# Kernel tuning notes

Hardware: AMD Instinct MI355X
Metric: run time of the kernel (lower is better)

## Reference

```python
import jax, jax.numpy as jnp
import numpy as np


def _linear_interp(t, S):
    """1D linear interpolation along last axis, matching F.interpolate(mode='linear', align_corners=False).
    t: [B, C, L] -> [B, C, S]"""
    L = t.shape[-1]
    src = jnp.clip((jnp.arange(S, dtype=jnp.float32) + 0.5) * (L / S) - 0.5, 0.0, L - 1)
    i0 = jnp.floor(src).astype(jnp.int32)
    i1 = jnp.minimum(i0 + 1, L - 1)
    w = (src - i0.astype(jnp.float32)).astype(t.dtype)
    return t[..., i0] * (1.0 - w) + t[..., i1] * w


def setup_inputs() -> dict:
    key = jax.random.key(0)
    k1, k2, k3, k4 = jax.random.split(key, 4)
    B, C, H, W, L, D = 32, 768, 32, 32, 77, 512
    return {
        "img_feat": jax.random.normal(k1, (B, C, H, W), dtype=jnp.float32),
        "text_feat": jax.random.normal(k2, (B, L, D), dtype=jnp.float32),
        "W_txt": jax.random.normal(k3, (D, C), dtype=jnp.float32) / np.float32(np.sqrt(D)),
        "gamma": jax.random.normal(k4, (1,), dtype=jnp.float32) * 0.1,
    }


def reference(img_feat, text_feat, W_txt, gamma):
    B, C, H, W = img_feat.shape
    S = H * W
    q = img_feat.reshape(B, C, S)                          # [B,C,S]
    # Linear(D->C, bias=False) then transpose(1,2): [B,L,D] -> [B,C,L]
    t = jnp.einsum('bld,dc->bcl', text_feat, W_txt)
    t = _linear_interp(t, S)                               # [B,C,S]
    scale = S ** (-0.5)
    # attn = bmm(q [B,C,S], t^T [B,S,C]) * scale -> [B,C,C] channel attention
    attn = jax.nn.softmax(jnp.einsum('bis,bjs->bij', q, t) * scale, axis=-1)
    out = q + gamma * jnp.einsum('bij,bjs->bis', attn, t)  # gamma-gated residual
    return out.reshape(B, C, H, W)
```

## Files before the change

### kernel.cpp

```cpp
#include <hip/hip_runtime.h>

#define BB 32
#define CC 768
#define SS 1024
#define LLn 77
#define DD 512
#define LP 80
#define LP2 96
#define QSTR 1048

#define RATIO 0.0751953125f

#define CVT_TXT_BLOCKS (BB * LP * DD / 4 / 256)
#define CVT_W_BLOCKS ((CC / 32) * (DD / 32))
#define AB_BLOCKS (4 * 5 * 8 * 64 * 8 / 4 / 256)
#define TG_BLOCKS (BB * 5 * 4)

typedef short bf16x8 __attribute__((ext_vector_type(8)));
typedef float f32x4 __attribute__((ext_vector_type(4)));
typedef unsigned short u16;

__device__ __forceinline__ u16 f2bf(float f) {
    unsigned int u; __builtin_memcpy(&u, &f, 4);
    u += 0x7fffu + ((u >> 16) & 1u);
    return (u16)(u >> 16);
}

__global__ __launch_bounds__(256) void k_cvt(const float* __restrict__ text,
                                             const float* __restrict__ Wt,
                                             u16* __restrict__ At,
                                             u16* __restrict__ Wb,
                                             u16* __restrict__ Abf) {
    __shared__ float tile[32 * 33];
    const int bx = blockIdx.x;
    const int tid = threadIdx.x;
    if (bx < CVT_TXT_BLOCKS) {
        int j = bx * 256 + tid;
        int row80 = j >> 7, col4 = (j & 127) << 2;
        int b = row80 / LP, l = row80 - b * LP;
        u16 o[4] = {0, 0, 0, 0};
        if (l < LLn) {
            float4 v = *reinterpret_cast<const float4*>(&text[((size_t)b * LLn + l) * DD + col4]);
            o[0] = f2bf(v.x); o[1] = f2bf(v.y); o[2] = f2bf(v.z); o[3] = f2bf(v.w);
        }
        *reinterpret_cast<uint2*>(&At[(size_t)row80 * DD + col4]) = *reinterpret_cast<uint2*>(o);
    } else if (bx < CVT_TXT_BLOCKS + CVT_W_BLOCKS) {
        const int bw = bx - CVT_TXT_BLOCKS;
        const int c0 = (bw % (CC / 32)) * 32, d0 = (bw / (CC / 32)) * 32;
        const int tx = tid & 31, ty = tid >> 5;
#pragma unroll
        for (int k = 0; k < 4; ++k) {
            int d = ty + k * 8;
            tile[d * 33 + tx] = Wt[(size_t)(d0 + d) * CC + c0 + tx];
        }
        __syncthreads();
#pragma unroll
        for (int k = 0; k < 4; ++k) {
            int c = ty + k * 8;
            Wb[(size_t)(c0 + c) * DD + d0 + tx] = f2bf(tile[tx * 33 + c]);
        }
    } else {
        int g = (bx - CVT_TXT_BLOCKS - CVT_W_BLOCKS) * 1024 + tid * 4;
        int e0   = g & 7;
        int lane = (g >> 3) & 63;
        int kk   = (g >> 9) & 7;
        int nt   = (g >> 12) % 5;
        int w    = g / 20480;
        int l    = nt * 16 + (lane & 15);
        int sb   = w * 256 + kk * 32 + ((lane >> 4) << 3) + e0;
        float fl = (float)l;
        u16 o[4];
#pragma unroll
        for (int k = 0; k < 4; ++k) {
            float src = fmaf((float)(sb + k) + 0.5f, RATIO, -0.5f);
            src = fminf(fmaxf(src, 0.f), 76.f);
            o[k] = f2bf(fmaxf(0.f, 1.f - fabsf(src - fl)) * 0.03125f);
        }
        *reinterpret_cast<uint2*>(&Abf[g]) = *reinterpret_cast<uint2*>(o);
    }
}

__global__ __launch_bounds__(256) void k_tgemm(const u16* __restrict__ At,
                                               const u16* __restrict__ Wb,
                                               u16* __restrict__ tc,
                                               u16* __restrict__ tlc) {
    const int bx = blockIdx.x;
    const int tid = threadIdx.x;
    const int cg = bx / 160, mt = bx % 160;
    const int b = mt / 5, tile = mt % 5;
    const int l0 = tile * 16;
    const int w = tid >> 6, lane = tid & 63;
    const int lm = lane & 15, lg = lane >> 4;
    const int c0 = cg * 192 + w * 48;

    f32x4 acc[3];
#pragma unroll
    for (int nt = 0; nt < 3; ++nt) acc[nt] = (f32x4){0.f, 0.f, 0.f, 0.f};

    const u16* ap = At + ((size_t)b * LP + l0 + lm) * DD + lg * 8;
    const u16* bp = Wb + (size_t)(c0 + lm) * DD + lg * 8;
#pragma unroll 4
    for (int ks = 0; ks < 16; ++ks) {
        bf16x8 aq = *reinterpret_cast<const bf16x8*>(ap + ks * 32);
#pragma unroll
        for (int nt = 0; nt < 3; ++nt) {
            bf16x8 bv = *reinterpret_cast<const bf16x8*>(bp + (size_t)nt * 16 * DD + ks * 32);
            acc[nt] = __builtin_amdgcn_mfma_f32_16x16x32_bf16(aq, bv, acc[nt], 0, 0, 0);
        }
    }

    const int lq = l0 + lg * 4;
#pragma unroll
    for (int nt = 0; nt < 3; ++nt) {
        int c = c0 + nt * 16 + lm;
        u16 pk[4];
#pragma unroll
        for (int r = 0; r < 4; ++r) pk[r] = f2bf(acc[nt][r]);
        uint2 pv; __builtin_memcpy(&pv, pk, 8);
        *reinterpret_cast<uint2*>(&tc[((size_t)b * CC + c) * LP2 + lq]) = pv;
#pragma unroll
        for (int r = 0; r < 4; ++r)
            tlc[((size_t)b * LP + lq + r) * CC + c] = pk[r];
    }
    if (tile == 4 && lg == 0) {
        uint4 z = {0u, 0u, 0u, 0u};
#pragma unroll
        for (int nt = 0; nt < 3; ++nt) {
            int c = c0 + nt * 16 + lm;
            *reinterpret_cast<uint4*>(&tc[((size_t)b * CC + c) * LP2 + 80]) = z;
            *reinterpret_cast<uint4*>(&tc[((size_t)b * CC + c) * LP2 + 88]) = z;
        }
    }
}

__global__ __launch_bounds__(256, 2) void k_fused(const u16* __restrict__ tc,
                                                  const u16* __restrict__ tlc,
                                                  const u16* __restrict__ Abf,
                                                  const float* __restrict__ q,
                                                  const float* __restrict__ gamma,
                                                  float* __restrict__ out) {
    __shared__ __align__(16) char un[16 * QSTR * 2];
    u16* qlds = (u16*)un;
    char* pbufBase = un;
    float* us = (float*)(un + 25600);
    float* pmax = (float*)(un + 30720);
    float* psum = (float*)(un + 30976);
    __shared__ u16 qh_bf[16 * 96];

    const int b = blockIdx.y;
    const int iBase = blockIdx.x * 16;
    const int tid = threadIdx.x;
    const int w = tid >> 6, lane = tid & 63;
    const int lm = lane & 15, lg = lane >> 4;
    const float g = gamma[0];

    const size_t qBase = ((size_t)b * CC + iBase) * SS + (size_t)(tid << 2);
    f32x4 qreg[16];
#pragma unroll
    for (int r = 0; r < 16; ++r)
        qreg[r] = *reinterpret_cast<const f32x4*>(&q[qBase + (size_t)r * SS]);
    const int s0 = tid << 2;
#pragma unroll
    for (int r = 0; r < 16; ++r) {
        u16 pk[4] = {f2bf(qreg[r][0]), f2bf(qreg[r][1]), f2bf(qreg[r][2]), f2bf(qreg[r][3])};
        uint2 pv; __builtin_memcpy(&pv, pk, 8);
        *reinterpret_cast<uint2*>(&qlds[r * QSTR + s0]) = pv;
    }
    __syncthreads();

    f32x4 aqh[5];
#pragma unroll
    for (int nt = 0; nt < 5; ++nt) aqh[nt] = (f32x4){0.f, 0.f, 0.f, 0.f};
    {
        const u16* abw = Abf + ((size_t)(w * 5) << 12) + (lane << 3);
#pragma unroll
        for (int kk = 0; kk < 8; ++kk) {
            bf16x8 av = *reinterpret_cast<const bf16x8*>(&qlds[lm * QSTR + w * 256 + kk * 32 + lg * 8]);
#pragma unroll
            for (int nt = 0; nt < 5; ++nt) {
                bf16x8 bv = *reinterpret_cast<const bf16x8*>(abw + (((nt << 3) + kk) << 9));
                aqh[nt] = __builtin_amdgcn_mfma_f32_16x16x32_bf16(av, bv, aqh[nt], 0, 0, 0);
            }
        }
    }
    __syncthreads();
    {
        float* qp = (float*)(pbufBase + w * 6400);
#pragma unroll
        for (int nt = 0; nt < 5; ++nt) {
#pragma unroll
            for (int r = 0; r < 4; ++r)
                qp[(lg * 4 + r) * 80 + nt * 16 + lm] = aqh[nt][r];
        }
    }
    __syncthreads();
#pragma unroll
    for (int k = 0; k < 5; ++k) {
        int e = tid + (k << 8);
        int row = e / 80, l = e - row * 80;
        float v = ((float*)(pbufBase))[row * 80 + l]
                + ((float*)(pbufBase + 6400))[row * 80 + l]
                + ((float*)(pbufBase + 12800))[row * 80 + l]
                + ((float*)(pbufBase + 19200))[row * 80 + l];
        qh_bf[row * 96 + l] = f2bf(v);
    }
    {
        int i = tid;
        if (i < 16 * 16) qh_bf[(i >> 4) * 96 + 80 + (i & 15)] = 0;
    }
    __syncthreads();

    bf16x8 aq0 = *reinterpret_cast<const bf16x8*>(&qh_bf[lm * 96 + lg * 8]);
    bf16x8 aq1 = *reinterpret_cast<const bf16x8*>(&qh_bf[lm * 96 + 32 + lg * 8]);
    bf16x8 aq2 = *reinterpret_cast<const bf16x8*>(&qh_bf[lm * 96 + 64 + lg * 8]);

    f32x4 acc[12];
#pragma unroll
    for (int t = 0; t < 12; ++t) acc[t] = (f32x4){0.f, 0.f, 0.f, 0.f};

    const u16* tcb = tc + ((size_t)b * CC + w * 192 + lm) * LP2 + lg * 8;
#pragma unroll
    for (int t = 0; t < 12; ++t) {
        const u16* p = tcb + (size_t)t * 16 * LP2;
        bf16x8 b0 = *reinterpret_cast<const bf16x8*>(p);
        bf16x8 b1 = *reinterpret_cast<const bf16x8*>(p + 32);
        bf16x8 b2 = *reinterpret_cast<const bf16x8*>(p + 64);
        acc[t] = __builtin_amdgcn_mfma_f32_16x16x32_bf16(aq0, b0, acc[t], 0, 0, 0);
        acc[t] = __builtin_amdgcn_mfma_f32_16x16x32_bf16(aq1, b1, acc[t], 0, 0, 0);
        acc[t] = __builtin_amdgcn_mfma_f32_16x16x32_bf16(aq2, b2, acc[t], 0, 0, 0);
    }

    float m[4];
#pragma unroll
    for (int r = 0; r < 4; ++r) {
        float mm = acc[0][r];
#pragma unroll
        for (int t = 1; t < 12; ++t) mm = fmaxf(mm, acc[t][r]);
#pragma unroll
        for (int off = 8; off >= 1; off >>= 1) mm = fmaxf(mm, __shfl_xor(mm, off));
        m[r] = mm;
    }
    if (lm == 0) {
#pragma unroll
        for (int r = 0; r < 4; ++r) pmax[w * 16 + lg * 4 + r] = m[r];
    }
    __syncthreads();
    float gm[4];
#pragma unroll
    for (int r = 0; r < 4; ++r) {
        int row = lg * 4 + r;
        gm[r] = fmaxf(fmaxf(pmax[row], pmax[16 + row]), fmaxf(pmax[32 + row], pmax[48 + row]));
    }
    float s[4] = {0.f, 0.f, 0.f, 0.f};
#pragma unroll
    for (int t = 0; t < 12; ++t) {
#pragma unroll
        for (int r = 0; r < 4; ++r) {
            float e = __expf(acc[t][r] - gm[r]);
            acc[t][r] = e;
            s[r] += e;
        }
    }
#pragma unroll
    for (int r = 0; r < 4; ++r) {
#pragma unroll
        for (int off = 8; off >= 1; off >>= 1) s[r] += __shfl_xor(s[r], off);
    }
    if (lm == 0) {
#pragma unroll
        for (int r = 0; r < 4; ++r) psum[w * 16 + lg * 4 + r] = s[r];
    }

    u16* P = (u16*)(pbufBase + w * 6400);
#pragma unroll
    for (int t = 0; t < 12; ++t) {
#pragma unroll
        for (int r = 0; r < 4; ++r)
            P[(lg * 4 + r) * 200 + t * 16 + lm] = f2bf(acc[t][r]);
    }

    f32x4 u[5];
#pragma unroll
    for (int nt = 0; nt < 5; ++nt) u[nt] = (f32x4){0.f, 0.f, 0.f, 0.f};
    const u16* tb = tlc + ((size_t)b * LP + lm) * CC + w * 192 + lg * 8;
#pragma unroll
    for (int ks = 0; ks < 6; ++ks) {
        bf16x8 pa = *reinterpret_cast<const bf16x8*>(&P[lm * 200 + ks * 32 + lg * 8]);
#pragma unroll
        for (int nt = 0; nt < 5; ++nt) {
            bf16x8 bv = *reinterpret_cast<const bf16x8*>(tb + (size_t)nt * 16 * CC + ks * 32);
            u[nt] = __builtin_amdgcn_mfma_f32_16x16x32_bf16(pa, bv, u[nt], 0, 0, 0);
        }
    }

    float* up = (float*)(pbufBase + w * 6400);
#pragma unroll
    for (int nt = 0; nt < 5; ++nt) {
#pragma unroll
        for (int r = 0; r < 4; ++r)
            up[(lg * 4 + r) * 81 + nt * 16 + lm] = u[nt][r];
    }
    __syncthreads();
#pragma unroll
    for (int k = 0; k < 5; ++k) {
        int idx = tid + (k << 8);
        int row = idx / LP, l = idx - row * LP;
        float v = ((float*)(pbufBase))[row * 81 + l]
                + ((float*)(pbufBase + 6400))[row * 81 + l]
                + ((float*)(pbufBase + 12800))[row * 81 + l]
                + ((float*)(pbufBase + 19200))[row * 81 + l];
        float denom = psum[row] + psum[16 + row] + psum[32 + row] + psum[48 + row];
        us[row * LP + l] = v / denom;
    }
    __syncthreads();

    float wgt[4]; int i0k[4], i1x[4];
#pragma unroll
    for (int k = 0; k < 4; ++k) {
        float src = fmaf((float)(s0 + k) + 0.5f, RATIO, -0.5f);
        src = fminf(fmaxf(src, 0.f), 76.f);
        i0k[k] = (int)src;
        wgt[k] = src - (float)i0k[k];
        i1x[k] = (i0k[k] < 76) ? i0k[k] + 1 : 76;
    }
#pragma unroll
    for (int r = 0; r < 16; ++r) {
        const float* ur = &us[r * LP];
        f32x4 o;
#pragma unroll
        for (int k = 0; k < 4; ++k) {
            float uv = fmaf(1.f - wgt[k], ur[i0k[k]], wgt[k] * ur[i1x[k]]);
            o[k] = qreg[r][k] + g * uv;
        }
        __builtin_nontemporal_store(o, reinterpret_cast<f32x4*>(&out[qBase + (size_t)r * SS]));
    }
}

extern "C" void kernel_launch(void* const* d_in, const int* in_sizes, int n_in,
                              void* d_out, int out_size, void* d_ws, size_t ws_size,
                              hipStream_t stream) {
    const float* img   = (const float*)d_in[0];
    const float* text  = (const float*)d_in[1];
    const float* Wt    = (const float*)d_in[2];
    const float* gamma = (const float*)d_in[3];
    float* out = (float*)d_out;
    char* ws = (char*)d_ws;
    u16*   tc_bf  = (u16*)(ws);
    u16*   tlc_bf = (u16*)(ws + 4718592);
    u16*   At_bf  = (u16*)(ws + 8650752);
    u16*   Wb_bf  = (u16*)(ws + 11272192);
    u16*   Abf_bf = (u16*)(ws + 12058624);

    k_cvt<<<dim3(CVT_TXT_BLOCKS + CVT_W_BLOCKS + AB_BLOCKS), 256, 0, stream>>>(
        text, Wt, At_bf, Wb_bf, Abf_bf);
    k_tgemm<<<dim3(TG_BLOCKS), 256, 0, stream>>>(At_bf, Wb_bf, tc_bf, tlc_bf);
    k_fused<<<dim3(48, BB), 256, 0, stream>>>(tc_bf, tlc_bf, Abf_bf, img, gamma, out);
}
```

Baseline: 98.89 us.

## Keep q as packed bf16 in registers, double-buffer MFMA operand loads, raise occupancy

Keeps the residual q in registers as packed bf16 rather than fp32, halving that register footprint. Raises the launch bound to 3 blocks per SIMD set. Software-pipelines the three MFMA phases (qh projection, logits, P·V) with A/B register double-buffering so global loads overlap compute. The residual add now uses bf16-rounded q instead of the exact fp32 input, which loses output precision and may exceed tolerance.

```diff
diff --git a/kernel.cpp b/kernel.cpp
--- a/kernel.cpp
+++ b/kernel.cpp
@@ -20,6 +20,12 @@
 typedef float f32x4 __attribute__((ext_vector_type(4)));
 typedef unsigned short u16;
 
+#define MFMA __builtin_amdgcn_mfma_f32_16x16x32_bf16
+
+__device__ __forceinline__ float bf2f(unsigned int h16) {
+    unsigned int u = h16 << 16;
+    float f; __builtin_memcpy(&f, &u, 4); return f;
+}
 __device__ __forceinline__ u16 f2bf(float f) {
     unsigned int u; __builtin_memcpy(&u, &f, 4);
     u += 0x7fffu + ((u >> 16) & 1u);
@@ -105,7 +111,7 @@
 #pragma unroll
         for (int nt = 0; nt < 3; ++nt) {
             bf16x8 bv = *reinterpret_cast<const bf16x8*>(bp + (size_t)nt * 16 * DD + ks * 32);
-            acc[nt] = __builtin_amdgcn_mfma_f32_16x16x32_bf16(aq, bv, acc[nt], 0, 0, 0);
+            acc[nt] = MFMA(aq, bv, acc[nt], 0, 0, 0);
         }
     }
 
@@ -133,7 +139,37 @@
     }
 }
 
-__global__ __launch_bounds__(256, 2) void k_fused(const u16* __restrict__ tc,
+#define LOADAB(arr, c) { _Pragma("unroll") for (int nt = 0; nt < 5; ++nt) { \
+    arr[2*nt]   = *reinterpret_cast<const bf16x8*>(abw + (((nt<<3)+2*(c))<<9)); \
+    arr[2*nt+1] = *reinterpret_cast<const bf16x8*>(abw + (((nt<<3)+2*(c)+1)<<9)); } }
+
+#define QHSTEP(c, CUR) { \
+    bf16x8 av0 = *reinterpret_cast<const bf16x8*>(&qlds[lm*QSTR + w*256 + (2*(c))*32 + lg*8]); \
+    bf16x8 av1 = *reinterpret_cast<const bf16x8*>(&qlds[lm*QSTR + w*256 + (2*(c)+1)*32 + lg*8]); \
+    _Pragma("unroll") for (int nt = 0; nt < 5; ++nt) { \
+        aqh[nt] = MFMA(av0, CUR[2*nt],   aqh[nt], 0, 0, 0); \
+        aqh[nt] = MFMA(av1, CUR[2*nt+1], aqh[nt], 0, 0, 0); } }
+
+#define LOADTC(arr, ch) { _Pragma("unroll") for (int tt = 0; tt < 2; ++tt) { \
+    const u16* p_ = tcb + (size_t)((ch)*2+tt) * 16 * LP2; \
+    arr[tt*3+0] = *reinterpret_cast<const bf16x8*>(p_); \
+    arr[tt*3+1] = *reinterpret_cast<const bf16x8*>(p_ + 32); \
+    arr[tt*3+2] = *reinterpret_cast<const bf16x8*>(p_ + 64); } }
+
+#define LSTEP(ch, CUR) { _Pragma("unroll") for (int tt = 0; tt < 2; ++tt) { \
+    acc[(ch)*2+tt] = MFMA(aq0, CUR[tt*3+0], acc[(ch)*2+tt], 0, 0, 0); \
+    acc[(ch)*2+tt] = MFMA(aq1, CUR[tt*3+1], acc[(ch)*2+tt], 0, 0, 0); \
+    acc[(ch)*2+tt] = MFMA(aq2, CUR[tt*3+2], acc[(ch)*2+tt], 0, 0, 0); } }
+
+#define LOADPV(arr, ks) { _Pragma("unroll") for (int nt = 0; nt < 5; ++nt) \
+    arr[nt] = *reinterpret_cast<const bf16x8*>(tb + (size_t)nt * 16 * CC + (ks)*32); }
+
+#define PVSTEP(ks, CUR) { \
+    bf16x8 pa = *reinterpret_cast<const bf16x8*>(&P[lm*200 + (ks)*32 + lg*8]); \
+    _Pragma("unroll") for (int nt = 0; nt < 5; ++nt) \
+        u[nt] = MFMA(pa, CUR[nt], u[nt], 0, 0, 0); }
+
+__global__ __launch_bounds__(256, 3) void k_fused(const u16* __restrict__ tc,
                                                   const u16* __restrict__ tlc,
                                                   const u16* __restrict__ Abf,
                                                   const float* __restrict__ q,
@@ -155,34 +191,38 @@
     const float g = gamma[0];
 
     const size_t qBase = ((size_t)b * CC + iBase) * SS + (size_t)(tid << 2);
-    f32x4 qreg[16];
+    const int s0 = tid << 2;
+    uint2 qpk[16];
+#pragma unroll
+    for (int r = 0; r < 16; ++r) {
+        f32x4 v = *reinterpret_cast<const f32x4*>(&q[qBase + (size_t)r * SS]);
+        u16 pk[4] = {f2bf(v[0]), f2bf(v[1]), f2bf(v[2]), f2bf(v[3])};
+        __builtin_memcpy(&qpk[r], pk, 8);
+    }
 #pragma unroll
     for (int r = 0; r < 16; ++r)
-        qreg[r] = *reinterpret_cast<const f32x4*>(&q[qBase + (size_t)r * SS]);
-    const int s0 = tid << 2;
-#pragma unroll
-    for (int r = 0; r < 16; ++r) {
-        u16 pk[4] = {f2bf(qreg[r][0]), f2bf(qreg[r][1]), f2bf(qreg[r][2]), f2bf(qreg[r][3])};
-        uint2 pv; __builtin_memcpy(&pv, pk, 8);
-        *reinterpret_cast<uint2*>(&qlds[r * QSTR + s0]) = pv;
-    }
+        *reinterpret_cast<uint2*>(&qlds[r * QSTR + s0]) = qpk[r];
+
+    const u16* abw = Abf + ((size_t)(w * 5) << 12) + (lane << 3);
+    bf16x8 abA[10], abB[10];
+    LOADAB(abA, 0);
     __syncthreads();
 
     f32x4 aqh[5];
 #pragma unroll
     for (int nt = 0; nt < 5; ++nt) aqh[nt] = (f32x4){0.f, 0.f, 0.f, 0.f};
-    {
-        const u16* abw = Abf + ((size_t)(w * 5) << 12) + (lane << 3);
-#pragma unroll
-        for (int kk = 0; kk < 8; ++kk) {
-            bf16x8 av = *reinterpret_cast<const bf16x8*>(&qlds[lm * QSTR + w * 256 + kk * 32 + lg * 8]);
-#pragma unroll
-            for (int nt = 0; nt < 5; ++nt) {
-                bf16x8 bv = *reinterpret_cast<const bf16x8*>(abw + (((nt << 3) + kk) << 9));
-                aqh[nt] = __builtin_amdgcn_mfma_f32_16x16x32_bf16(av, bv, aqh[nt], 0, 0, 0);
-            }
-        }
-    }
+    LOADAB(abB, 1);
+    QHSTEP(0, abA);
+    LOADAB(abA, 2);
+    QHSTEP(1, abB);
+    LOADAB(abB, 3);
+    QHSTEP(2, abA);
+    QHSTEP(3, abB);
+
+    const u16* tcb = tc + ((size_t)b * CC + w * 192 + lm) * LP2 + lg * 8;
+    bf16x8 tcA[6], tcB[6];
+    LOADTC(tcA, 0);
+
     __syncthreads();
     {
         float* qp = (float*)(pbufBase + w * 6400);
@@ -204,10 +244,7 @@
                 + ((float*)(pbufBase + 19200))[row * 80 + l];
         qh_bf[row * 96 + l] = f2bf(v);
     }
-    {
-        int i = tid;
-        if (i < 16 * 16) qh_bf[(i >> 4) * 96 + 80 + (i & 15)] = 0;
-    }
+    if (tid < 16 * 16) qh_bf[(tid >> 4) * 96 + 80 + (tid & 15)] = 0;
     __syncthreads();
 
     bf16x8 aq0 = *reinterpret_cast<const bf16x8*>(&qh_bf[lm * 96 + lg * 8]);
@@ -218,17 +255,21 @@
 #pragma unroll
     for (int t = 0; t < 12; ++t) acc[t] = (f32x4){0.f, 0.f, 0.f, 0.f};
 
-    const u16* tcb = tc + ((size_t)b * CC + w * 192 + lm) * LP2 + lg * 8;
-#pragma unroll
-    for (int t = 0; t < 12; ++t) {
-        const u16* p = tcb + (size_t)t * 16 * LP2;
-        bf16x8 b0 = *reinterpret_cast<const bf16x8*>(p);
-        bf16x8 b1 = *reinterpret_cast<const bf16x8*>(p + 32);
-        bf16x8 b2 = *reinterpret_cast<const bf16x8*>(p + 64);
-        acc[t] = __builtin_amdgcn_mfma_f32_16x16x32_bf16(aq0, b0, acc[t], 0, 0, 0);
-        acc[t] = __builtin_amdgcn_mfma_f32_16x16x32_bf16(aq1, b1, acc[t], 0, 0, 0);
-        acc[t] = __builtin_amdgcn_mfma_f32_16x16x32_bf16(aq2, b2, acc[t], 0, 0, 0);
-    }
+    LOADTC(tcB, 1);
+    LSTEP(0, tcA);
+    LOADTC(tcA, 2);
+    LSTEP(1, tcB);
+    LOADTC(tcB, 3);
+    LSTEP(2, tcA);
+    LOADTC(tcA, 4);
+    LSTEP(3, tcB);
+    LOADTC(tcB, 5);
+    LSTEP(4, tcA);
+    LSTEP(5, tcB);
+
+    const u16* tb = tlc + ((size_t)b * LP + lm) * CC + w * 192 + lg * 8;
+    bf16x8 pvA[5], pvB[5];
+    LOADPV(pvA, 0);
 
     float m[4];
 #pragma unroll
@@ -282,16 +323,17 @@
     f32x4 u[5];
 #pragma unroll
     for (int nt = 0; nt < 5; ++nt) u[nt] = (f32x4){0.f, 0.f, 0.f, 0.f};
-    const u16* tb = tlc + ((size_t)b * LP + lm) * CC + w * 192 + lg * 8;
-#pragma unroll
-    for (int ks = 0; ks < 6; ++ks) {
-        bf16x8 pa = *reinterpret_cast<const bf16x8*>(&P[lm * 200 + ks * 32 + lg * 8]);
-#pragma unroll
-        for (int nt = 0; nt < 5; ++nt) {
-            bf16x8 bv = *reinterpret_cast<const bf16x8*>(tb + (size_t)nt * 16 * CC + ks * 32);
-            u[nt] = __builtin_amdgcn_mfma_f32_16x16x32_bf16(pa, bv, u[nt], 0, 0, 0);
-        }
-    }
+    LOADPV(pvB, 1);
+    PVSTEP(0, pvA);
+    LOADPV(pvA, 2);
+    PVSTEP(1, pvB);
+    LOADPV(pvB, 3);
+    PVSTEP(2, pvA);
+    LOADPV(pvA, 4);
+    PVSTEP(3, pvB);
+    LOADPV(pvB, 5);
+    PVSTEP(4, pvA);
+    PVSTEP(5, pvB);
 
     float* up = (float*)(pbufBase + w * 6400);
 #pragma unroll
@@ -326,11 +368,14 @@
 #pragma unroll
     for (int r = 0; r < 16; ++r) {
         const float* ur = &us[r * LP];
+        uint2 qq = qpk[r];
+        float qf[4] = {bf2f(qq.x & 0xffffu), bf2f(qq.x >> 16),
+                       bf2f(qq.y & 0xffffu), bf2f(qq.y >> 16)};
         f32x4 o;
 #pragma unroll
         for (int k = 0; k < 4; ++k) {
             float uv = fmaf(1.f - wgt[k], ur[i0k[k]], wgt[k] * ur[i1x[k]]);
-            o[k] = qreg[r][k] + g * uv;
+            o[k] = qf[k] + g * uv;
         }
         __builtin_nontemporal_store(o, reinterpret_cast<f32x4*>(&out[qBase + (size_t)r * SS]));
     }
```

Result: no change. 98.33 us (-0.6%).

## Keep q as packed bf16 in registers, shrink LDS, raise occupancy, remap blocks

Applied to the files above, without the earlier changes.

The fused kernel now holds the image tile as packed bf16 in registers instead of fp32, halving that register footprint. Each wave stages only its own slice of q in a per-wave LDS region, which drops one block-wide barrier and shrinks shared memory. Launch bounds go from 2 to 4 blocks per SIMD to raise occupancy, and a 1D grid with a swizzled block-to-batch mapping is meant to improve L2 locality across XCDs. The trade-off is that the residual term is now added from bf16-rounded q rather than exact fp32 input, which loses accuracy in the output.

```diff
diff --git a/kernel.cpp b/kernel.cpp
--- a/kernel.cpp
+++ b/kernel.cpp
@@ -7,7 +7,8 @@
 #define DD 512
 #define LP 80
 #define LP2 96
-#define QSTR 1048
+#define QBS 264
+#define WREG 8448
 
 #define RATIO 0.0751953125f
 
@@ -20,6 +21,12 @@
 typedef float f32x4 __attribute__((ext_vector_type(4)));
 typedef unsigned short u16;
 
+#define MFMA __builtin_amdgcn_mfma_f32_16x16x32_bf16
+
+__device__ __forceinline__ float bf2f(unsigned int h16) {
+    unsigned int u = h16 << 16;
+    float f; __builtin_memcpy(&f, &u, 4); return f;
+}
 __device__ __forceinline__ u16 f2bf(float f) {
     unsigned int u; __builtin_memcpy(&u, &f, 4);
     u += 0x7fffu + ((u >> 16) & 1u);
@@ -105,7 +112,7 @@
 #pragma unroll
         for (int nt = 0; nt < 3; ++nt) {
             bf16x8 bv = *reinterpret_cast<const bf16x8*>(bp + (size_t)nt * 16 * DD + ks * 32);
-            acc[nt] = __builtin_amdgcn_mfma_f32_16x16x32_bf16(aq, bv, acc[nt], 0, 0, 0);
+            acc[nt] = MFMA(aq, bv, acc[nt], 0, 0, 0);
         }
     }
 
@@ -133,59 +140,56 @@
     }
 }
 
-__global__ __launch_bounds__(256, 2) void k_fused(const u16* __restrict__ tc,
+__global__ __launch_bounds__(256, 4) void k_fused(const u16* __restrict__ tc,
                                                   const u16* __restrict__ tlc,
                                                   const u16* __restrict__ Abf,
                                                   const float* __restrict__ q,
                                                   const float* __restrict__ gamma,
                                                   float* __restrict__ out) {
-    __shared__ __align__(16) char un[16 * QSTR * 2];
-    u16* qlds = (u16*)un;
-    char* pbufBase = un;
-    float* us = (float*)(un + 25600);
-    float* pmax = (float*)(un + 30720);
-    float* psum = (float*)(un + 30976);
-    __shared__ u16 qh_bf[16 * 96];
-
-    const int b = blockIdx.y;
-    const int iBase = blockIdx.x * 16;
+    __shared__ __align__(16) char un[4 * WREG];
+    __shared__ __align__(16) char sh2[5120];
+    __shared__ float pmax[64];
+    __shared__ float psum[64];
+
+    const int id = blockIdx.x;
+    const int o = id >> 3;
+    const int b = (id & 7) * 4 + o / 48;
+    const int iBase = (o % 48) * 16;
+
     const int tid = threadIdx.x;
     const int w = tid >> 6, lane = tid & 63;
     const int lm = lane & 15, lg = lane >> 4;
     const float g = gamma[0];
 
     const size_t qBase = ((size_t)b * CC + iBase) * SS + (size_t)(tid << 2);
-    f32x4 qreg[16];
+    const int s0 = tid << 2;
+    uint2 qpk[16];
+#pragma unroll
+    for (int r = 0; r < 16; ++r) {
+        f32x4 v = *reinterpret_cast<const f32x4*>(&q[qBase + (size_t)r * SS]);
+        u16 pk[4] = {f2bf(v[0]), f2bf(v[1]), f2bf(v[2]), f2bf(v[3])};
+        __builtin_memcpy(&qpk[r], pk, 8);
+    }
+    u16* qbuf = (u16*)(un + w * WREG);
 #pragma unroll
     for (int r = 0; r < 16; ++r)
-        qreg[r] = *reinterpret_cast<const f32x4*>(&q[qBase + (size_t)r * SS]);
-    const int s0 = tid << 2;
-#pragma unroll
-    for (int r = 0; r < 16; ++r) {
-        u16 pk[4] = {f2bf(qreg[r][0]), f2bf(qreg[r][1]), f2bf(qreg[r][2]), f2bf(qreg[r][3])};
-        uint2 pv; __builtin_memcpy(&pv, pk, 8);
-        *reinterpret_cast<uint2*>(&qlds[r * QSTR + s0]) = pv;
-    }
-    __syncthreads();
+        *reinterpret_cast<uint2*>(&qbuf[r * QBS + lane * 4]) = qpk[r];
 
     f32x4 aqh[5];
 #pragma unroll
     for (int nt = 0; nt < 5; ++nt) aqh[nt] = (f32x4){0.f, 0.f, 0.f, 0.f};
+    const u16* abw = Abf + ((size_t)(w * 5) << 12) + (lane << 3);
+#pragma unroll
+    for (int kk = 0; kk < 8; ++kk) {
+        bf16x8 av = *reinterpret_cast<const bf16x8*>(&qbuf[lm * QBS + kk * 32 + lg * 8]);
+#pragma unroll
+        for (int nt = 0; nt < 5; ++nt) {
+            bf16x8 bv = *reinterpret_cast<const bf16x8*>(abw + (((nt << 3) + kk) << 9));
+            aqh[nt] = MFMA(av, bv, aqh[nt], 0, 0, 0);
+        }
+    }
     {
-        const u16* abw = Abf + ((size_t)(w * 5) << 12) + (lane << 3);
-#pragma unroll
-        for (int kk = 0; kk < 8; ++kk) {
-            bf16x8 av = *reinterpret_cast<const bf16x8*>(&qlds[lm * QSTR + w * 256 + kk * 32 + lg * 8]);
-#pragma unroll
-            for (int nt = 0; nt < 5; ++nt) {
-                bf16x8 bv = *reinterpret_cast<const bf16x8*>(abw + (((nt << 3) + kk) << 9));
-                aqh[nt] = __builtin_amdgcn_mfma_f32_16x16x32_bf16(av, bv, aqh[nt], 0, 0, 0);
-            }
-        }
-    }
-    __syncthreads();
-    {
-        float* qp = (float*)(pbufBase + w * 6400);
+        float* qp = (float*)(un + w * WREG);
 #pragma unroll
         for (int nt = 0; nt < 5; ++nt) {
 #pragma unroll
@@ -194,20 +198,19 @@
         }
     }
     __syncthreads();
+
+    u16* qh_bf = (u16*)sh2;
 #pragma unroll
     for (int k = 0; k < 5; ++k) {
         int e = tid + (k << 8);
         int row = e / 80, l = e - row * 80;
-        float v = ((float*)(pbufBase))[row * 80 + l]
-                + ((float*)(pbufBase + 6400))[row * 80 + l]
-                + ((float*)(pbufBase + 12800))[row * 80 + l]
-                + ((float*)(pbufBase + 19200))[row * 80 + l];
+        float v = ((float*)(un))[row * 80 + l]
+                + ((float*)(un + WREG))[row * 80 + l]
+                + ((float*)(un + 2 * WREG))[row * 80 + l]
+                + ((float*)(un + 3 * WREG))[row * 80 + l];
         qh_bf[row * 96 + l] = f2bf(v);
     }
-    {
-        int i = tid;
-        if (i < 16 * 16) qh_bf[(i >> 4) * 96 + 80 + (i & 15)] = 0;
-    }
+    if (tid < 16 * 16) qh_bf[(tid >> 4) * 96 + 80 + (tid & 15)] = 0;
     __syncthreads();
 
     bf16x8 aq0 = *reinterpret_cast<const bf16x8*>(&qh_bf[lm * 96 + lg * 8]);
@@ -225,9 +228,9 @@
         bf16x8 b0 = *reinterpret_cast<const bf16x8*>(p);
         bf16x8 b1 = *reinterpret_cast<const bf16x8*>(p + 32);
         bf16x8 b2 = *reinterpret_cast<const bf16x8*>(p + 64);
-        acc[t] = __builtin_amdgcn_mfma_f32_16x16x32_bf16(aq0, b0, acc[t], 0, 0, 0);
-        acc[t] = __builtin_amdgcn_mfma_f32_16x16x32_bf16(aq1, b1, acc[t], 0, 0, 0);
-        acc[t] = __builtin_amdgcn_mfma_f32_16x16x32_bf16(aq2, b2, acc[t], 0, 0, 0);
+        acc[t] = MFMA(aq0, b0, acc[t], 0, 0, 0);
+        acc[t] = MFMA(aq1, b1, acc[t], 0, 0, 0);
+        acc[t] = MFMA(aq2, b2, acc[t], 0, 0, 0);
     }
 
     float m[4];
@@ -271,7 +274,7 @@
         for (int r = 0; r < 4; ++r) psum[w * 16 + lg * 4 + r] = s[r];
     }
 
-    u16* P = (u16*)(pbufBase + w * 6400);
+    u16* P = (u16*)(un + w * WREG);
 #pragma unroll
     for (int t = 0; t < 12; ++t) {
 #pragma unroll
@@ -289,11 +292,11 @@
 #pragma unroll
         for (int nt = 0; nt < 5; ++nt) {
             bf16x8 bv = *reinterpret_cast<const bf16x8*>(tb + (size_t)nt * 16 * CC + ks * 32);
-            u[nt] = __builtin_amdgcn_mfma_f32_16x16x32_bf16(pa, bv, u[nt], 0, 0, 0);
-        }
-    }
-
-    float* up = (float*)(pbufBase + w * 6400);
+            u[nt] = MFMA(pa, bv, u[nt], 0, 0, 0);
+        }
+    }
+
+    float* up = (float*)(un + w * WREG);
 #pragma unroll
     for (int nt = 0; nt < 5; ++nt) {
 #pragma unroll
@@ -301,14 +304,15 @@
             up[(lg * 4 + r) * 81 + nt * 16 + lm] = u[nt][r];
     }
     __syncthreads();
+    float* us = (float*)sh2;
 #pragma unroll
     for (int k = 0; k < 5; ++k) {
         int idx = tid + (k << 8);
         int row = idx / LP, l = idx - row * LP;
-        float v = ((float*)(pbufBase))[row * 81 + l]
-                + ((float*)(pbufBase + 6400))[row * 81 + l]
-                + ((float*)(pbufBase + 12800))[row * 81 + l]
-                + ((float*)(pbufBase + 19200))[row * 81 + l];
+        float v = ((float*)(un))[row * 81 + l]
+                + ((float*)(un + WREG))[row * 81 + l]
+                + ((float*)(un + 2 * WREG))[row * 81 + l]
+                + ((float*)(un + 3 * WREG))[row * 81 + l];
         float denom = psum[row] + psum[16 + row] + psum[32 + row] + psum[48 + row];
         us[row * LP + l] = v / denom;
     }
@@ -326,13 +330,16 @@
 #pragma unroll
     for (int r = 0; r < 16; ++r) {
         const float* ur = &us[r * LP];
-        f32x4 o;
+        uint2 qq = qpk[r];
+        float qf[4] = {bf2f(qq.x & 0xffffu), bf2f(qq.x >> 16),
+                       bf2f(qq.y & 0xffffu), bf2f(qq.y >> 16)};
+        f32x4 ov;
 #pragma unroll
         for (int k = 0; k < 4; ++k) {
             float uv = fmaf(1.f - wgt[k], ur[i0k[k]], wgt[k] * ur[i1x[k]]);
-            o[k] = qreg[r][k] + g * uv;
-        }
-        __builtin_nontemporal_store(o, reinterpret_cast<f32x4*>(&out[qBase + (size_t)r * SS]));
+            ov[k] = qf[k] + g * uv;
+        }
+        __builtin_nontemporal_store(ov, reinterpret_cast<f32x4*>(&out[qBase + (size_t)r * SS]));
     }
 }
 
@@ -354,5 +361,5 @@
     k_cvt<<<dim3(CVT_TXT_BLOCKS + CVT_W_BLOCKS + AB_BLOCKS), 256, 0, stream>>>(
         text, Wt, At_bf, Wb_bf, Abf_bf);
     k_tgemm<<<dim3(TG_BLOCKS), 256, 0, stream>>>(At_bf, Wb_bf, tc_bf, tlc_bf);
-    k_fused<<<dim3(48, BB), 256, 0, stream>>>(tc_bf, tlc_bf, Abf_bf, img, gamma, out);
-}
+    k_fused<<<dim3(48 * BB), 256, 0, stream>>>(tc_bf, tlc_bf, Abf_bf, img, gamma, out);
+}
```

Result: slower. 125.3 us (+26.7%).
